# Kernel optimization log

Measured on AMD Instinct MI355X. Metric: run time of the kernel, lower is better.

The kernel has to match this reference:

```python
import math
import jax, jax.numpy as jnp
import numpy as np

H, W = 24, 24
N = H * W
D = 1024
B = 32
MAX_ITERS = 6

# 9 relative neighbor offsets (3x3 window, row-major)
_REL = np.array([[-1, -1], [-1, 0], [-1, 1], [0, -1], [0, 0], [0, 1], [1, -1], [1, 0], [1, 1]])


def _neighbor_cols():
    y, x = np.meshgrid(np.arange(H), np.arange(W), indexing='ij')
    ny = np.clip(y[None] + _REL[:, 0, None, None], 0, H - 1)  # [9,H,W]
    nx = np.clip(x[None] + _REL[:, 1, None, None], 0, W - 1)
    return jnp.asarray((ny * W + nx).reshape(9, N))  # [9,N]


def setup_inputs() -> dict:
    key = jax.random.key(0)
    ks = jax.random.split(key, 8)
    return {
        'tok2d': jax.random.normal(ks[0], (B, N + 1, D), dtype=jnp.float32),
        'dw_w': jax.random.normal(ks[1], (D, 1, 3, 3), dtype=jnp.float32) * 0.02,
        'pw_w': jax.random.normal(ks[2], (9, D, 1, 1), dtype=jnp.float32) * 0.02,
        'pw_b': jnp.zeros((9,), dtype=jnp.float32),
        'q_w': jax.random.normal(ks[3], (D, D), dtype=jnp.float32) * 0.02,
        'q_b': jax.random.normal(ks[4], (D,), dtype=jnp.float32) * 0.02,
        'v_w': jax.random.normal(ks[5], (D, D), dtype=jnp.float32) * 0.02,
        'v_b': jax.random.normal(ks[6], (D,), dtype=jnp.float32) * 0.02,
        'K': 256,
        'MAX_TOKENS': 128,
    }


def _affinity_head(patch2d, dw_w, pw_w, pw_b):
    # patch2d: [B,H,W,D] -> Q: [B,H,W,9]
    x = jnp.transpose(patch2d, (0, 3, 1, 2))  # NCHW
    x = jax.lax.conv_general_dilated(
        x, dw_w, window_strides=(1, 1), padding='SAME',
        feature_group_count=D,
        dimension_numbers=('NCHW', 'OIHW', 'NCHW'))
    x = jnp.einsum('bdhw,od->bohw', x, pw_w[:, :, 0, 0]) + pw_b[None, :, None, None]
    return jax.nn.softmax(jnp.transpose(x, (0, 2, 3, 1)), axis=-1)


def _build_token_affinity(Q):
    # Q: [B,H,W,9] -> A: [B,N,N] via 9 shifted-neighbor scatters
    cols = _neighbor_cols()                                   # [9,N]
    rows = jnp.broadcast_to(jnp.arange(N)[None, :], (9, N))   # [9,N]
    vals = jnp.moveaxis(Q.reshape(-1, N, 9), -1, 1).reshape(-1, 9 * N)  # [B,9*N]
    A = jnp.zeros((Q.shape[0], N, N), dtype=Q.dtype)
    return A.at[:, rows.reshape(-1), cols.reshape(-1)].add(vals)


def _cluster_roots(A):
    roots = jnp.argmax(A, axis=-1)  # [B,N]
    for _ in range(MAX_ITERS):      # pointer jumping (idempotent once converged)
        roots = jnp.take_along_axis(roots, roots, axis=1)
    return roots


def _cluster_centers(E, roots, K):
    b = E.shape[0]
    bidx = jnp.arange(b)[:, None]
    centers_sum = jnp.zeros_like(E).at[bidx, roots].add(E)          # [B,N,D]
    counts = jnp.zeros(E.shape[:2], E.dtype).at[bidx, roots].add(1.0)  # [B,N]
    _, topk_idx = jax.lax.top_k(counts, K)
    ord_idx = jnp.sort(topk_idx, axis=1)
    cs = jnp.take_along_axis(centers_sum, ord_idx[:, :, None], axis=1)
    cnt = jnp.take_along_axis(counts, ord_idx, axis=1)
    C = cs / jnp.clip(cnt, 1.0, None)[:, :, None]
    return C, cnt


def reference(tok2d, dw_w, pw_w, pw_b, q_w, q_b, v_w, v_b, K, MAX_TOKENS):
    cls_tok = tok2d[:, :1, :]                 # [B,1,D]
    patch = tok2d[:, 1:, :]                   # [B,N,D]
    Q = _affinity_head(patch.reshape(-1, H, W, D), dw_w, pw_w, pw_b)
    A = _build_token_affinity(Q)
    roots = _cluster_roots(A)
    C, cnt = _cluster_centers(patch, roots, K)
    Q_cls = cls_tok @ q_w.T + q_b             # [B,1,D]
    K_v = C @ v_w.T + v_b                     # [B,K,D]
    scores = jnp.einsum('bod,bkd->bk', Q_cls, K_v) / math.sqrt(D)
    valid = jnp.where(cnt > 0, scores, -jnp.inf)
    m = min(MAX_TOKENS, C.shape[1])
    _, idx = jax.lax.top_k(valid, m)
    idx_sorted = jnp.sort(idx, axis=-1)
    return jnp.take_along_axis(C, idx_sorted[:, :, None], axis=1)  # [B,m,D]
```

## Files before the change

kernel.cpp:

```cpp
#include <hip/hip_runtime.h>
#include <math.h>

#define Hh 24
#define Ww 24
#define Nn 576
#define Dd 1024
#define Bb 32
#define Kk 256
#define Mm 128
#define TOKSTRIDE (577 * 1024)

#define R0_OFF 0
#define P_OFF 2944
#define QC_OFF 3776
#define U_OFF 4800
#define T_OFF 5824

__device__ __forceinline__ float* batch_base(float* out, int b) {
  return out + (size_t)b * Mm * Dd;
}

__device__ __forceinline__ float wave_sum_dpp(float x) {
  int y;
  y = __builtin_amdgcn_update_dpp(0, __float_as_int(x), 0x111, 0xf, 0xf, true);
  x += __int_as_float(y);
  y = __builtin_amdgcn_update_dpp(0, __float_as_int(x), 0x112, 0xf, 0xf, true);
  x += __int_as_float(y);
  y = __builtin_amdgcn_update_dpp(0, __float_as_int(x), 0x114, 0xf, 0xf, true);
  x += __int_as_float(y);
  y = __builtin_amdgcn_update_dpp(0, __float_as_int(x), 0x118, 0xf, 0xf, true);
  x += __int_as_float(y);
  y = __builtin_amdgcn_update_dpp(0, __float_as_int(x), 0x142, 0xa, 0xf, true);
  x += __int_as_float(y);
  y = __builtin_amdgcn_update_dpp(0, __float_as_int(x), 0x143, 0xc, 0xf, true);
  x += __int_as_float(y);
  return x;
}

__device__ __forceinline__ float row_sum_dpp(float x) {
  int y;
  y = __builtin_amdgcn_update_dpp(0, __float_as_int(x), 0x111, 0xf, 0xf, true);
  x += __int_as_float(y);
  y = __builtin_amdgcn_update_dpp(0, __float_as_int(x), 0x112, 0xf, 0xf, true);
  x += __int_as_float(y);
  y = __builtin_amdgcn_update_dpp(0, __float_as_int(x), 0x114, 0xf, 0xf, true);
  x += __int_as_float(y);
  y = __builtin_amdgcn_update_dpp(0, __float_as_int(x), 0x118, 0xf, 0xf, true);
  x += __int_as_float(y);
  return x;
}

__global__ __launch_bounds__(256) void qcls_kernel(
    const float* __restrict__ tok2d, const float* __restrict__ q_w,
    const float* __restrict__ q_b, float* __restrict__ outb) {
  int dp = blockIdx.x;
  int wave = threadIdx.x >> 6;
  int lane = threadIdx.x & 63;
  float4 qv[4];
#pragma unroll
  for (int i = 0; i < 4; i++)
    qv[i] = *(const float4*)(q_w + (size_t)dp * Dd + lane * 4 + 256 * i);
  float qb = q_b[dp];
#pragma unroll 2
  for (int bb = 0; bb < 8; bb++) {
    int b = wave * 8 + bb;
    const float* cls = tok2d + (size_t)b * TOKSTRIDE;
    float a = 0.f;
#pragma unroll
    for (int i = 0; i < 4; i++) {
      float4 cv = *(const float4*)(cls + lane * 4 + 256 * i);
      a += qv[i].x * cv.x + qv[i].y * cv.y + qv[i].z * cv.z + qv[i].w * cv.w;
    }
    a = wave_sum_dpp(a);
    if (lane == 63) batch_base(outb, b)[QC_OFF + dp] = a + qb;
  }
}

__global__ __launch_bounds__(256) void u_t_kernel(const float* __restrict__ v_w,
                                                  const float* __restrict__ v_b,
                                                  float* __restrict__ outb) {
  int b = blockIdx.x >> 3;
  int s = blockIdx.x & 7;
  int tid = threadIdx.x;
  int dl = tid & 31;
  int g = tid >> 5;
  float* basef = batch_base(outb, b);
  __shared__ float qs[Dd];
  __shared__ float4 part[8][32];
  __shared__ float sh[256];
  for (int i = tid; i < Dd; i += 256) qs[i] = basef[QC_OFF + i];
  __syncthreads();
  int d0 = s * 128 + dl * 4;
  float4 a = make_float4(0.f, 0.f, 0.f, 0.f);
#pragma unroll 4
  for (int dpl = 0; dpl < 128; dpl++) {
    int dp = g * 128 + dpl;
    float4 vv = *(const float4*)(v_w + (size_t)dp * Dd + d0);
    float qq = qs[dp];
    a.x += qq * vv.x; a.y += qq * vv.y; a.z += qq * vv.z; a.w += qq * vv.w;
  }
  part[g][dl] = a;
  __syncthreads();
  if (tid < 32) {
    float4 u = make_float4(0.f, 0.f, 0.f, 0.f);
#pragma unroll
    for (int c = 0; c < 8; c++) {
      float4 v = part[c][tid];
      u.x += v.x; u.y += v.y; u.z += v.z; u.w += v.w;
    }
    *(float4*)(basef + U_OFF + s * 128 + tid * 4) = u;
  }

  if (s == 0) {
    float aa = 0.f;
    for (int i = tid; i < Dd; i += 256) aa += qs[i] * v_b[i];
    sh[tid] = aa;
    __syncthreads();
    for (int st = 128; st > 0; st >>= 1) {
      if (tid < st) sh[tid] += sh[tid + st];
      __syncthreads();
    }
    if (tid == 0) basef[T_OFF] = sh[0];
  }
}

__global__ __launch_bounds__(256, 3) void affinity_p_root_kernel(
    const float* __restrict__ tok2d, const float* __restrict__ dw_w,
    const float* __restrict__ pw_w, const float* __restrict__ pw_b,
    float* __restrict__ outb) {
  int wave = threadIdx.x >> 6;
  int lane = threadIdx.x & 63;
  int blk = (blockIdx.x & 7) * (Bb * Hh * 3 / 8) + (blockIdx.x >> 3);
  int b = blk / (Hh * 3);
  int rem = blk % (Hh * 3);
  int y = rem / 3;
  int x0 = (rem % 3) * 8;
  int d0 = wave * 256 + lane * 4;
  const float* patch = tok2d + (size_t)b * TOKSTRIDE + Dd;
  float* basef = batch_base(outb, b);

  __shared__ float red[8 * 167 + 8];

  union { float4 v[9]; float f[36]; } w;
  const float4* dwp = (const float4*)(dw_w + (size_t)d0 * 9);
#pragma unroll
  for (int j = 0; j < 9; j++) w.v[j] = dwp[j];
  float4 u4 = *(const float4*)(basef + U_OFF + d0);

  float4 cc[8];
  float pacc[8];
#pragma unroll
  for (int t = 0; t < 8; t++) {
    cc[t] = make_float4(0.f, 0.f, 0.f, 0.f);
    pacc[t] = 0.f;
  }
#pragma unroll
  for (int ky = 0; ky < 3; ky++) {
    int yy = y + ky - 1;
    if (yy < 0 || yy >= Hh) continue;
    const float* prow = patch + (size_t)(yy * Ww) * Dd + d0;
    float4 wrow[10];
    wrow[0] = make_float4(0.f, 0.f, 0.f, 0.f);
    if (x0 > 0) wrow[0] = *(const float4*)(prow + (size_t)(x0 - 1) * Dd);
#pragma unroll
    for (int j = 1; j < 9; j++)
      wrow[j] = *(const float4*)(prow + (size_t)(x0 - 1 + j) * Dd);
    wrow[9] = make_float4(0.f, 0.f, 0.f, 0.f);
    if (x0 + 8 < Ww) wrow[9] = *(const float4*)(prow + (size_t)(x0 + 8) * Dd);
    int kA = ky * 3, kB = ky * 3 + 1, kC = ky * 3 + 2;
#pragma unroll
    for (int t = 0; t < 8; t++) {
      cc[t].x += wrow[t].x * w.f[kA] + wrow[t + 1].x * w.f[kB] +
                 wrow[t + 2].x * w.f[kC];
      cc[t].y += wrow[t].y * w.f[9 + kA] + wrow[t + 1].y * w.f[9 + kB] +
                 wrow[t + 2].y * w.f[9 + kC];
      cc[t].z += wrow[t].z * w.f[18 + kA] + wrow[t + 1].z * w.f[18 + kB] +
                 wrow[t + 2].z * w.f[18 + kC];
      cc[t].w += wrow[t].w * w.f[27 + kA] + wrow[t + 1].w * w.f[27 + kB] +
                 wrow[t + 2].w * w.f[27 + kC];
      if (ky == 1)
        pacc[t] = wrow[t + 1].x * u4.x + wrow[t + 1].y * u4.y +
                  wrow[t + 1].z * u4.z + wrow[t + 1].w * u4.w;
    }
  }

  __builtin_amdgcn_sched_barrier(0);

  float4 pw[9];
#pragma unroll
  for (int o = 0; o < 9; o++)
    pw[o] = *(const float4*)(pw_w + (size_t)o * Dd + d0);

#pragma unroll
  for (int t = 0; t < 8; t++) {
    float acc[10];
#pragma unroll
    for (int o = 0; o < 9; o++) {
      acc[o] = cc[t].x * pw[o].x + cc[t].y * pw[o].y + cc[t].z * pw[o].z +
               cc[t].w * pw[o].w;
    }
    acc[9] = pacc[t];
#pragma unroll
    for (int o = 0; o < 10; o++) acc[o] = row_sum_dpp(acc[o]);
    if ((lane & 15) == 15) {
      int r = wave * 4 + (lane >> 4);
#pragma unroll
      for (int o = 0; o < 10; o++) red[t * 167 + r * 10 + o] = acc[o];
    }
  }
  __syncthreads();

  if (lane < 2) {
    int t = wave * 2 + lane;
    int x = x0 + t;
    int n = y * Ww + x;
    float l[10];
#pragma unroll
    for (int o = 0; o < 10; o++) l[o] = 0.f;
    for (int r = 0; r < 16; r++) {
#pragma unroll
      for (int o = 0; o < 10; o++) l[o] += red[t * 167 + r * 10 + o];
    }
    float q[9];
    float mx = -INFINITY;
#pragma unroll
    for (int o = 0; o < 9; o++) {
      l[o] += pw_b[o];
      mx = fmaxf(mx, l[o]);
    }
    float ssum = 0.f;
#pragma unroll
    for (int o = 0; o < 9; o++) {
      q[o] = expf(l[o] - mx);
      ssum += q[o];
    }
#pragma unroll
    for (int o = 0; o < 9; o++) q[o] = q[o] / ssum;

    int colv[9];
#pragma unroll
    for (int o = 0; o < 9; o++) {
      int dy = o / 3 - 1, dx = o % 3 - 1;
      int ny = min(max(y + dy, 0), Hh - 1);
      int nx = min(max(x + dx, 0), Ww - 1);
      colv[o] = ny * Ww + nx;
    }
    float best = -1.f;
    int bcol = 1 << 30;
#pragma unroll
    for (int o = 0; o < 9; o++) {
      float v = 0.f;
#pragma unroll
      for (int oo = 0; oo < 9; oo++)
        v = (colv[oo] == colv[o]) ? v + q[oo] : v;
      if (v > best || (v == best && colv[o] < bcol)) {
        best = v;
        bcol = colv[o];
      }
    }
    ((int*)basef)[R0_OFF + n] = bcol;
    basef[P_OFF + n] = l[9];
  }
}

__global__ __launch_bounds__(576) void cluster_scores_plan_kernel(
    float* __restrict__ outb) {
  int b = blockIdx.x;
  int n = threadIdx.x;
  float* basef = batch_base(outb, b);
  int* base = (int*)basef;
  __shared__ int ra[Nn], rb[Nn], scnt[Nn], soff[Nn], smem[Nn];
  __shared__ float sp[Nn];
  __shared__ int s_ord[Kk], s_cnt[Kk], sel[Kk], s_out[Mm];
  __shared__ float ss[Kk];
  ra[n] = base[R0_OFF + n];
  sp[n] = basef[P_OFF + n];
  scnt[n] = 0;
  __syncthreads();
  for (int it = 0; it < 6; it++) {
    rb[n] = ra[ra[n]];
    __syncthreads();
    ra[n] = rb[n];
    __syncthreads();
  }
  int r = ra[n];
  atomicAdd(&scnt[r], 1);
  __syncthreads();

  soff[n] = scnt[n];
  __syncthreads();
  for (int s = 1; s < Nn; s <<= 1) {
    int v = (n >= s) ? soff[n - s] : 0;
    __syncthreads();
    soff[n] += v;
    __syncthreads();
  }
  int offr = soff[r] - scnt[r];
  int rk = 0;
  for (int m = 0; m < n; m++) rk += (ra[m] == r);
  smem[offr + rk] = n;

  int cn = scnt[n];
  int rank = 0;
  for (int m = 0; m < Nn; m++) {
    int cm = scnt[m];
    rank += (cm > cn) || (cm == cn && m < n);
  }
  int sl = (rank < Kk) ? 1 : 0;
  rb[n] = sl;
  __syncthreads();
  for (int s = 1; s < Nn; s <<= 1) {
    int v = (n >= s) ? rb[n - s] : 0;
    __syncthreads();
    rb[n] += v;
    __syncthreads();
  }
  if (sl) {
    int pos = rb[n] - 1;
    s_ord[pos] = n;
    s_cnt[pos] = cn;
  }
  __syncthreads();

  if (n < Kk) {
    int idx = s_ord[n];
    int c = s_cnt[n];
    float s;
    if (c > 0) {
      int off = soff[idx] - scnt[idx];
      float sum = 0.f;
      for (int j = 0; j < c; j++) sum += sp[smem[off + j]];
      s = (sum / (float)c + basef[T_OFF]) * (1.0f / 32.0f);
    } else {
      s = -INFINITY;
    }
    ss[n] = s;
  }
  __syncthreads();

  if (n < Kk) {
    float vk = ss[n];
    int rank2 = 0;
    for (int m = 0; m < Kk; m++) {
      float vm = ss[m];
      rank2 += (vm > vk) || (vm == vk && m < n);
    }
    sel[n] = (rank2 < Mm) ? 1 : 0;
  }
  __syncthreads();
  if (n < Kk && sel[n]) {
    int pos = 0;
    for (int m = 0; m < n; m++) pos += sel[m];
    s_out[pos] = n;
  }
  __syncthreads();

  int w9 = n >> 6, lane = n & 63;
  for (int kp = w9; kp < Mm; kp += 9) {
    int k = s_out[kp];
    int kidx = s_ord[k];
    int kc = s_cnt[k];
    int koff = soff[kidx] - scnt[kidx];
    int* row = base + kp * Dd;
    if (lane == 0) row[0] = kc;
    for (int j = lane; j < kc; j += 64) row[1 + j] = smem[koff + j];
  }
}

__global__ __launch_bounds__(256) void output_kernel(
    const float* __restrict__ tok2d, float* __restrict__ outb) {
  int blk = blockIdx.x;
  int b = blk / Mm;
  int tid = threadIdx.x;
  float* rowf = outb + (size_t)blk * Dd;
  int* rowi = (int*)rowf;
  __shared__ int s_c;
  __shared__ int s_m[Nn];
  if (tid == 0) s_c = rowi[0];
  __syncthreads();
  int c = s_c;
  for (int j = tid; j < c; j += 256) s_m[j] = rowi[1 + j];
  __syncthreads();
  const float* patch = tok2d + (size_t)b * TOKSTRIDE + Dd;
  int d0 = tid * 4;
  float4 acc = make_float4(0.f, 0.f, 0.f, 0.f);
  for (int j = 0; j < c; j++) {
    float4 rv = *(const float4*)(patch + (size_t)s_m[j] * Dd + d0);
    acc.x += rv.x; acc.y += rv.y; acc.z += rv.z; acc.w += rv.w;
  }
  float inv = 1.0f / (float)max(c, 1);
  *(float4*)(rowf + d0) =
      make_float4(acc.x * inv, acc.y * inv, acc.z * inv, acc.w * inv);
}

extern "C" void kernel_launch(void* const* d_in, const int* in_sizes, int n_in,
                              void* d_out, int out_size, void* d_ws,
                              size_t ws_size, hipStream_t stream) {
  const float* tok2d = (const float*)d_in[0];
  const float* dw_w = (const float*)d_in[1];
  const float* pw_w = (const float*)d_in[2];
  const float* pw_b = (const float*)d_in[3];
  const float* q_w = (const float*)d_in[4];
  const float* q_b = (const float*)d_in[5];
  const float* v_w = (const float*)d_in[6];
  const float* v_b = (const float*)d_in[7];
  float* out = (float*)d_out;
  (void)d_ws; (void)ws_size;

  qcls_kernel<<<dim3(Dd), dim3(256), 0, stream>>>(tok2d, q_w, q_b, out);
  u_t_kernel<<<dim3(Bb * 8), dim3(256), 0, stream>>>(v_w, v_b, out);
  affinity_p_root_kernel<<<dim3(Bb * Hh * 3), dim3(256), 0, stream>>>(
      tok2d, dw_w, pw_w, pw_b, out);
  cluster_scores_plan_kernel<<<dim3(Bb), dim3(Nn), 0, stream>>>(out);
  output_kernel<<<dim3(Bb * Mm), dim3(256), 0, stream>>>(tok2d, out);
}
```

Baseline: 234.4 us.

## Fuse dependent kernel pairs using global atomic counters instead of launch boundaries

```diff
diff --git a/kernel.cpp b/kernel.cpp
--- a/kernel.cpp
+++ b/kernel.cpp
@@ -50,44 +50,66 @@
   return x;
 }
 
-__global__ __launch_bounds__(256) void qcls_kernel(
+__device__ __forceinline__ void publish_done(unsigned int* c) {
+  if (threadIdx.x == 0) {
+    __threadfence();
+    atomicAdd(c, 1u);
+  }
+}
+__device__ __forceinline__ void wait_done(unsigned int* c, unsigned int tgt) {
+  if (threadIdx.x == 0) {
+    while (__hip_atomic_load(c, __ATOMIC_RELAXED, __HIP_MEMORY_SCOPE_AGENT) <
+           tgt)
+      __builtin_amdgcn_s_sleep(8);
+    __threadfence();
+  }
+  __syncthreads();
+}
+
+__global__ __launch_bounds__(256) void qcls_ut_fused(
     const float* __restrict__ tok2d, const float* __restrict__ q_w,
-    const float* __restrict__ q_b, float* __restrict__ outb) {
-  int dp = blockIdx.x;
-  int wave = threadIdx.x >> 6;
-  int lane = threadIdx.x & 63;
-  float4 qv[4];
-#pragma unroll
-  for (int i = 0; i < 4; i++)
-    qv[i] = *(const float4*)(q_w + (size_t)dp * Dd + lane * 4 + 256 * i);
-  float qb = q_b[dp];
+    const float* __restrict__ q_b, const float* __restrict__ v_w,
+    const float* __restrict__ v_b, float* __restrict__ outb,
+    unsigned int* __restrict__ cnt) {
+  __shared__ float qs[Dd];
+  __shared__ float4 part[8][32];
+  __shared__ float sh[256];
+  int tid = threadIdx.x;
+
+  if (blockIdx.x < 1024) {
+    int dp = blockIdx.x;
+    int wave = tid >> 6;
+    int lane = tid & 63;
+    float4 qv[4];
+#pragma unroll
+    for (int i = 0; i < 4; i++)
+      qv[i] = *(const float4*)(q_w + (size_t)dp * Dd + lane * 4 + 256 * i);
+    float qb = q_b[dp];
 #pragma unroll 2
-  for (int bb = 0; bb < 8; bb++) {
-    int b = wave * 8 + bb;
-    const float* cls = tok2d + (size_t)b * TOKSTRIDE;
-    float a = 0.f;
-#pragma unroll
-    for (int i = 0; i < 4; i++) {
-      float4 cv = *(const float4*)(cls + lane * 4 + 256 * i);
-      a += qv[i].x * cv.x + qv[i].y * cv.y + qv[i].z * cv.z + qv[i].w * cv.w;
-    }
-    a = wave_sum_dpp(a);
-    if (lane == 63) batch_base(outb, b)[QC_OFF + dp] = a + qb;
-  }
-}
-
-__global__ __launch_bounds__(256) void u_t_kernel(const float* __restrict__ v_w,
-                                                  const float* __restrict__ v_b,
-                                                  float* __restrict__ outb) {
-  int b = blockIdx.x >> 3;
-  int s = blockIdx.x & 7;
-  int tid = threadIdx.x;
+    for (int bb = 0; bb < 8; bb++) {
+      int b = wave * 8 + bb;
+      const float* cls = tok2d + (size_t)b * TOKSTRIDE;
+      float a = 0.f;
+#pragma unroll
+      for (int i = 0; i < 4; i++) {
+        float4 cv = *(const float4*)(cls + lane * 4 + 256 * i);
+        a += qv[i].x * cv.x + qv[i].y * cv.y + qv[i].z * cv.z + qv[i].w * cv.w;
+      }
+      a = wave_sum_dpp(a);
+      if (lane == 63) batch_base(outb, b)[QC_OFF + dp] = a + qb;
+    }
+    __syncthreads();
+    publish_done(&cnt[0]);
+    return;
+  }
+
+  wait_done(&cnt[0], 1024u);
+  int idx = blockIdx.x - 1024;
+  int b = idx >> 3;
+  int s = idx & 7;
   int dl = tid & 31;
   int g = tid >> 5;
   float* basef = batch_base(outb, b);
-  __shared__ float qs[Dd];
-  __shared__ float4 part[8][32];
-  __shared__ float sh[256];
   for (int i = tid; i < Dd; i += 256) qs[i] = basef[QC_OFF + i];
   __syncthreads();
   int d0 = s * 128 + dl * 4;
@@ -110,7 +132,6 @@
     }
     *(float4*)(basef + U_OFF + s * 128 + tid * 4) = u;
   }
-
   if (s == 0) {
     float aa = 0.f;
     for (int i = tid; i < Dd; i += 256) aa += qs[i] * v_b[i];
@@ -263,13 +284,225 @@
   }
 }
 
+__global__ __launch_bounds__(576) void csp_out_fused(
+    const float* __restrict__ tok2d, float* __restrict__ outb,
+    unsigned int* __restrict__ cnt) {
+  __shared__ int ra[Nn], rb2[Nn], scnt[Nn], soff[Nn], smem[Nn];
+  __shared__ float sp[Nn];
+  __shared__ int s_ord[Kk], s_cnt[Kk], sel[Kk], s_out[Mm];
+  __shared__ float ss[Kk];
+  __shared__ int s_c;
+  int n = threadIdx.x;
+
+  if (blockIdx.x < 32) {
+    int b = blockIdx.x;
+    float* basef = batch_base(outb, b);
+    int* base = (int*)basef;
+    ra[n] = base[R0_OFF + n];
+    sp[n] = basef[P_OFF + n];
+    scnt[n] = 0;
+    __syncthreads();
+    for (int it = 0; it < 6; it++) {
+      rb2[n] = ra[ra[n]];
+      __syncthreads();
+      ra[n] = rb2[n];
+      __syncthreads();
+    }
+    int r = ra[n];
+    atomicAdd(&scnt[r], 1);
+    __syncthreads();
+
+    soff[n] = scnt[n];
+    __syncthreads();
+    for (int s = 1; s < Nn; s <<= 1) {
+      int v = (n >= s) ? soff[n - s] : 0;
+      __syncthreads();
+      soff[n] += v;
+      __syncthreads();
+    }
+    int offr = soff[r] - scnt[r];
+    int rk = 0;
+    for (int m = 0; m < n; m++) rk += (ra[m] == r);
+    smem[offr + rk] = n;
+
+    int cn = scnt[n];
+    int rank = 0;
+    for (int m = 0; m < Nn; m++) {
+      int cm = scnt[m];
+      rank += (cm > cn) || (cm == cn && m < n);
+    }
+    int sl = (rank < Kk) ? 1 : 0;
+    rb2[n] = sl;
+    __syncthreads();
+    for (int s = 1; s < Nn; s <<= 1) {
+      int v = (n >= s) ? rb2[n - s] : 0;
+      __syncthreads();
+      rb2[n] += v;
+      __syncthreads();
+    }
+    if (sl) {
+      int pos = rb2[n] - 1;
+      s_ord[pos] = n;
+      s_cnt[pos] = cn;
+    }
+    __syncthreads();
+
+    if (n < Kk) {
+      int idx = s_ord[n];
+      int c = s_cnt[n];
+      float s;
+      if (c > 0) {
+        int off = soff[idx] - scnt[idx];
+        float sum = 0.f;
+        for (int j = 0; j < c; j++) sum += sp[smem[off + j]];
+        s = (sum / (float)c + basef[T_OFF]) * (1.0f / 32.0f);
+      } else {
+        s = -INFINITY;
+      }
+      ss[n] = s;
+    }
+    __syncthreads();
+
+    if (n < Kk) {
+      float vk = ss[n];
+      int rank2 = 0;
+      for (int m = 0; m < Kk; m++) {
+        float vm = ss[m];
+        rank2 += (vm > vk) || (vm == vk && m < n);
+      }
+      sel[n] = (rank2 < Mm) ? 1 : 0;
+    }
+    __syncthreads();
+    if (n < Kk && sel[n]) {
+      int pos = 0;
+      for (int m = 0; m < n; m++) pos += sel[m];
+      s_out[pos] = n;
+    }
+    __syncthreads();
+
+    int w9 = n >> 6, lane = n & 63;
+    for (int kp = w9; kp < Mm; kp += 9) {
+      int k = s_out[kp];
+      int kidx = s_ord[k];
+      int kc = s_cnt[k];
+      int koff = soff[kidx] - scnt[kidx];
+      int* row = base + kp * Dd;
+      if (lane == 0) row[0] = kc;
+      for (int j = lane; j < kc; j += 64) row[1 + j] = smem[koff + j];
+    }
+    __syncthreads();
+    publish_done(&cnt[1]);
+    return;
+  }
+
+  wait_done(&cnt[1], 32u);
+  int base_row = (blockIdx.x - 32) * 8;
+  int b = base_row >> 7;
+  const float* patch = tok2d + (size_t)b * TOKSTRIDE + Dd;
+  for (int rr = 0; rr < 8; rr++) {
+    int row = base_row + rr;
+    float* rowf = outb + (size_t)row * Dd;
+    int* rowi = (int*)rowf;
+    if (n == 0) s_c = rowi[0];
+    __syncthreads();
+    int c = s_c;
+    for (int j = n; j < c; j += 576) smem[j] = rowi[1 + j];
+    __syncthreads();
+    if (n < 512) {
+      int d0 = n * 2;
+      float2 acc = make_float2(0.f, 0.f);
+      for (int j = 0; j < c; j++) {
+        float2 rv = *(const float2*)(patch + (size_t)smem[j] * Dd + d0);
+        acc.x += rv.x;
+        acc.y += rv.y;
+      }
+      float inv = 1.0f / (float)max(c, 1);
+      *(float2*)(rowf + d0) = make_float2(acc.x * inv, acc.y * inv);
+    }
+    __syncthreads();
+  }
+}
+
+__global__ __launch_bounds__(256) void qcls_kernel(
+    const float* __restrict__ tok2d, const float* __restrict__ q_w,
+    const float* __restrict__ q_b, float* __restrict__ outb) {
+  int dp = blockIdx.x;
+  int wave = threadIdx.x >> 6;
+  int lane = threadIdx.x & 63;
+  float4 qv[4];
+#pragma unroll
+  for (int i = 0; i < 4; i++)
+    qv[i] = *(const float4*)(q_w + (size_t)dp * Dd + lane * 4 + 256 * i);
+  float qb = q_b[dp];
+#pragma unroll 2
+  for (int bb = 0; bb < 8; bb++) {
+    int b = wave * 8 + bb;
+    const float* cls = tok2d + (size_t)b * TOKSTRIDE;
+    float a = 0.f;
+#pragma unroll
+    for (int i = 0; i < 4; i++) {
+      float4 cv = *(const float4*)(cls + lane * 4 + 256 * i);
+      a += qv[i].x * cv.x + qv[i].y * cv.y + qv[i].z * cv.z + qv[i].w * cv.w;
+    }
+    a = wave_sum_dpp(a);
+    if (lane == 63) batch_base(outb, b)[QC_OFF + dp] = a + qb;
+  }
+}
+
+__global__ __launch_bounds__(256) void u_t_kernel(const float* __restrict__ v_w,
+                                                  const float* __restrict__ v_b,
+                                                  float* __restrict__ outb) {
+  int b = blockIdx.x >> 3;
+  int s = blockIdx.x & 7;
+  int tid = threadIdx.x;
+  int dl = tid & 31;
+  int g = tid >> 5;
+  float* basef = batch_base(outb, b);
+  __shared__ float qs[Dd];
+  __shared__ float4 part[8][32];
+  __shared__ float sh[256];
+  for (int i = tid; i < Dd; i += 256) qs[i] = basef[QC_OFF + i];
+  __syncthreads();
+  int d0 = s * 128 + dl * 4;
+  float4 a = make_float4(0.f, 0.f, 0.f, 0.f);
+#pragma unroll 4
+  for (int dpl = 0; dpl < 128; dpl++) {
+    int dp = g * 128 + dpl;
+    float4 vv = *(const float4*)(v_w + (size_t)dp * Dd + d0);
+    float qq = qs[dp];
+    a.x += qq * vv.x; a.y += qq * vv.y; a.z += qq * vv.z; a.w += qq * vv.w;
+  }
+  part[g][dl] = a;
+  __syncthreads();
+  if (tid < 32) {
+    float4 u = make_float4(0.f, 0.f, 0.f, 0.f);
+#pragma unroll
+    for (int c = 0; c < 8; c++) {
+      float4 v = part[c][tid];
+      u.x += v.x; u.y += v.y; u.z += v.z; u.w += v.w;
+    }
+    *(float4*)(basef + U_OFF + s * 128 + tid * 4) = u;
+  }
+  if (s == 0) {
+    float aa = 0.f;
+    for (int i = tid; i < Dd; i += 256) aa += qs[i] * v_b[i];
+    sh[tid] = aa;
+    __syncthreads();
+    for (int st = 128; st > 0; st >>= 1) {
+      if (tid < st) sh[tid] += sh[tid + st];
+      __syncthreads();
+    }
+    if (tid == 0) basef[T_OFF] = sh[0];
+  }
+}
+
 __global__ __launch_bounds__(576) void cluster_scores_plan_kernel(
     float* __restrict__ outb) {
   int b = blockIdx.x;
   int n = threadIdx.x;
   float* basef = batch_base(outb, b);
   int* base = (int*)basef;
-  __shared__ int ra[Nn], rb[Nn], scnt[Nn], soff[Nn], smem[Nn];
+  __shared__ int ra[Nn], rb2[Nn], scnt[Nn], soff[Nn], smem[Nn];
   __shared__ float sp[Nn];
   __shared__ int s_ord[Kk], s_cnt[Kk], sel[Kk], s_out[Mm];
   __shared__ float ss[Kk];
@@ -278,15 +511,14 @@
   scnt[n] = 0;
   __syncthreads();
   for (int it = 0; it < 6; it++) {
-    rb[n] = ra[ra[n]];
-    __syncthreads();
-    ra[n] = rb[n];
+    rb2[n] = ra[ra[n]];
+    __syncthreads();
+    ra[n] = rb2[n];
     __syncthreads();
   }
   int r = ra[n];
   atomicAdd(&scnt[r], 1);
   __syncthreads();
-
   soff[n] = scnt[n];
   __syncthreads();
   for (int s = 1; s < Nn; s <<= 1) {
@@ -299,7 +531,6 @@
   int rk = 0;
   for (int m = 0; m < n; m++) rk += (ra[m] == r);
   smem[offr + rk] = n;
-
   int cn = scnt[n];
   int rank = 0;
   for (int m = 0; m < Nn; m++) {
@@ -307,21 +538,20 @@
     rank += (cm > cn) || (cm == cn && m < n);
   }
   int sl = (rank < Kk) ? 1 : 0;
-  rb[n] = sl;
+  rb2[n] = sl;
   __syncthreads();
   for (int s = 1; s < Nn; s <<= 1) {
-    int v = (n >= s) ? rb[n - s] : 0;
-    __syncthreads();
-    rb[n] += v;
+    int v = (n >= s) ? rb2[n - s] : 0;
+    __syncthreads();
+    rb2[n] += v;
     __syncthreads();
   }
   if (sl) {
-    int pos = rb[n] - 1;
+    int pos = rb2[n] - 1;
     s_ord[pos] = n;
     s_cnt[pos] = cn;
   }
   __syncthreads();
-
   if (n < Kk) {
     int idx = s_ord[n];
     int c = s_cnt[n];
@@ -337,7 +567,6 @@
     ss[n] = s;
   }
   __syncthreads();
-
   if (n < Kk) {
     float vk = ss[n];
     int rank2 = 0;
@@ -354,7 +583,6 @@
     s_out[pos] = n;
   }
   __syncthreads();
-
   int w9 = n >> 6, lane = n & 63;
   for (int kp = w9; kp < Mm; kp += 9) {
     int k = s_out[kp];
@@ -405,12 +633,21 @@
   const float* v_w = (const float*)d_in[6];
   const float* v_b = (const float*)d_in[7];
   float* out = (float*)d_out;
-  (void)d_ws; (void)ws_size;
-
-  qcls_kernel<<<dim3(Dd), dim3(256), 0, stream>>>(tok2d, q_w, q_b, out);
-  u_t_kernel<<<dim3(Bb * 8), dim3(256), 0, stream>>>(v_w, v_b, out);
-  affinity_p_root_kernel<<<dim3(Bb * Hh * 3), dim3(256), 0, stream>>>(
-      tok2d, dw_w, pw_w, pw_b, out);
-  cluster_scores_plan_kernel<<<dim3(Bb), dim3(Nn), 0, stream>>>(out);
-  output_kernel<<<dim3(Bb * Mm), dim3(256), 0, stream>>>(tok2d, out);
-}
+
+  if (ws_size >= 64) {
+    unsigned int* cnt = (unsigned int*)d_ws;
+    hipMemsetAsync(d_ws, 0, 64, stream);
+    qcls_ut_fused<<<dim3(1280), dim3(256), 0, stream>>>(tok2d, q_w, q_b, v_w,
+                                                        v_b, out, cnt);
+    affinity_p_root_kernel<<<dim3(Bb * Hh * 3), dim3(256), 0, stream>>>(
+        tok2d, dw_w, pw_w, pw_b, out);
+    csp_out_fused<<<dim3(32 + 512), dim3(576), 0, stream>>>(tok2d, out, cnt);
+  } else {
+    qcls_kernel<<<dim3(Dd), dim3(256), 0, stream>>>(tok2d, q_w, q_b, out);
+    u_t_kernel<<<dim3(Bb * 8), dim3(256), 0, stream>>>(v_w, v_b, out);
+    affinity_p_root_kernel<<<dim3(Bb * Hh * 3), dim3(256), 0, stream>>>(
+        tok2d, dw_w, pw_w, pw_b, out);
+    cluster_scores_plan_kernel<<<dim3(Bb), dim3(Nn), 0, stream>>>(out);
+    output_kernel<<<dim3(Bb * Mm), dim3(256), 0, stream>>>(tok2d, out);
+  }
+}
```

After: 309.8 us. 32.2% more time.
